# Performance work log

Hardware: AMD Instinct MI355X
Metric: run time of the kernel (lower is better)

The kernel has to match this reference:

```python
import jax, jax.numpy as jnp
import numpy as np

MASK_ID = -100
L, D, HID, NH = 10, 768, 3072, 12
DH = D // NH
REACH = 2  # (sliding_window_size - 1) // 2 with window 5


def _layernorm(x, g, b, eps=1e-5):
    mu = x.mean(-1, keepdims=True)
    var = ((x - mu) ** 2).mean(-1, keepdims=True)
    return (x - mu) * jax.lax.rsqrt(var + eps) * g + b


def _adaln(x, temb, w, bb, g, be):
    # AdaLayerNormShiftScale: linear(silu(temb)) -> (scale, shift)
    e = jax.nn.silu(temb) @ w + bb
    scale, shift = jnp.split(e, 2, axis=-1)
    return _layernorm(x, g, be) * (1.0 + scale) + shift


def _timestep_emb(t):
    half = D // 2
    exponent = -np.log(10000.0) * jnp.arange(half, dtype=jnp.float32) / (half - 1.0)
    freq = jnp.exp(exponent)  # [half]
    emb = t.astype(jnp.float32)[..., None] * freq  # [b,s,half]
    return jnp.concatenate([jnp.sin(emb), jnp.cos(emb)], axis=-1)  # [b,s,D]


def setup_inputs():
    key = jax.random.key(0)
    ks = jax.random.split(key, 16)
    b, s = 4, 1024
    # packed token ids: 4 samples of 256 tokens (16x16 grid), last 64 tokens padding
    idx = np.arange(s)
    sid = idx // 256
    hpos = (idx % 256) // 16
    wpos = idx % 16
    sid = np.where(idx >= 960, MASK_ID, sid)
    tok = np.stack([sid, hpos, wpos], axis=-1)  # [s,3]
    token_ids = jnp.asarray(np.broadcast_to(tok, (b, s, 3)).copy(), dtype=jnp.int32)
    t = jax.random.randint(ks[0], (b, 1), 0, L + 1).astype(jnp.int32)
    t = jnp.broadcast_to(t, (b, s))

    def w(k, shape):
        return jax.random.normal(k, shape, jnp.float32) * 0.02

    return dict(
        x=jax.random.normal(ks[1], (b, s, D), jnp.float32),
        t=t,
        token_ids=token_ids,
        proj_in_w=w(ks[2], (D, D)), proj_in_b=jnp.zeros((D,), jnp.float32),
        h_emb=w(ks[3], (64, D)), w_emb=w(ks[4], (64, D)),
        adaln1_w=w(ks[5], (L, D, 2 * D)), adaln1_b=jnp.zeros((L, 2 * D), jnp.float32),
        ln1_g=jnp.ones((L, D), jnp.float32), ln1_b=jnp.zeros((L, D), jnp.float32),
        qkv_w=w(ks[6], (L, D, 3 * D)), qkv_b=jnp.zeros((L, 3 * D), jnp.float32),
        o_w=w(ks[7], (L, D, D)), o_b=jnp.zeros((L, D), jnp.float32),
        adaln2_w=w(ks[8], (L, D, 2 * D)), adaln2_b=jnp.zeros((L, 2 * D), jnp.float32),
        ln2_g=jnp.ones((L, D), jnp.float32), ln2_b=jnp.zeros((L, D), jnp.float32),
        fc1_w=w(ks[9], (L, D, HID)), fc1_b=jnp.zeros((L, HID), jnp.float32),
        fc2_w=w(ks[10], (L, HID, D)), fc2_b=jnp.zeros((L, D), jnp.float32),
        nout_w=w(ks[11], (D, 2 * D)), nout_b=jnp.zeros((2 * D,), jnp.float32),
        nout_g=jnp.ones((D,), jnp.float32), nout_beta=jnp.zeros((D,), jnp.float32),
    )


def _encoder(x, t, token_ids, proj_in_w, proj_in_b, h_emb, w_emb,
             adaln1_w, adaln1_b, ln1_g, ln1_b, qkv_w, qkv_b, o_w, o_b,
             adaln2_w, adaln2_b, ln2_g, ln2_b, fc1_w, fc1_b, fc2_w, fc2_b,
             nout_w, nout_b, nout_g, nout_beta):
    b, s, _ = x.shape
    sample_ids = token_ids[..., 0]          # [b,s]
    pos = token_ids[..., 1:]                # [b,s,2]
    x = x @ proj_in_w + proj_in_b
    x = x + h_emb[pos[..., 0]] + w_emb[pos[..., 1]]

    # block-sparse mask: same packed sample, Chebyshev sliding window, no padding queries
    same = sample_ids[:, :, None] == sample_ids[:, None, :]              # [b,s,s]
    cheby = jnp.abs(pos[:, :, None, :] - pos[:, None, :, :]).max(-1)      # [b,s,s]
    notpad_q = (sample_ids != MASK_ID)[:, :, None]
    mask = same & (cheby <= REACH) & notpad_q                             # [b,s,s]
    row_valid = mask.any(-1)[..., None]                                   # [b,s,1]

    temb = _timestep_emb(t)  # [b,s,D]
    scale = 1.0 / np.sqrt(DH)
    for i in range(L):
        h1 = _adaln(x, temb, adaln1_w[i], adaln1_b[i], ln1_g[i], ln1_b[i])
        qkv = h1 @ qkv_w[i] + qkv_b[i]
        q, k, v = jnp.split(qkv, 3, axis=-1)
        q = q.reshape(b, s, NH, DH)
        k = k.reshape(b, s, NH, DH)
        v = v.reshape(b, s, NH, DH)
        scores = jnp.einsum('bqhd,bkhd->bhqk', q, k) * scale
        scores = jnp.where(mask[:, None], scores, -1e30)
        attn = jax.nn.softmax(scores, axis=-1)
        o = jnp.einsum('bhqk,bkhd->bqhd', attn, v).reshape(b, s, D)
        o = jnp.where(row_valid, o, 0.0)  # fully-masked (padding) rows -> 0
        x = x + o @ o_w[i] + o_b[i]
        h2 = _adaln(x, temb, adaln2_w[i], adaln2_b[i], ln2_g[i], ln2_b[i])
        x = x + jax.nn.gelu(h2 @ fc1_w[i] + fc1_b[i], approximate=False) @ fc2_w[i] + fc2_b[i]
    x = _adaln(x, temb, nout_w, nout_b, nout_g, nout_beta)
    return x


def reference(x, t, token_ids, proj_in_w, proj_in_b, h_emb, w_emb,
              adaln1_w, adaln1_b, ln1_g, ln1_b, qkv_w, qkv_b, o_w, o_b,
              adaln2_w, adaln2_b, ln2_g, ln2_b, fc1_w, fc1_b, fc2_w, fc2_b,
              nout_w, nout_b, nout_g, nout_beta):
    return _encoder(x, t, token_ids, proj_in_w, proj_in_b, h_emb, w_emb,
                    adaln1_w, adaln1_b, ln1_g, ln1_b, qkv_w, qkv_b, o_w, o_b,
                    adaln2_w, adaln2_b, ln2_g, ln2_b, fc1_w, fc1_b, fc2_w, fc2_b,
                    nout_w, nout_b, nout_g, nout_beta)
```

## Files before the change

### kernel.cpp

```cpp
#include <hip/hip_runtime.h>
#include <hip/hip_bf16.h>
#include <math.h>

#define MASK_ID (-100)
#define SEQ 1024
#define BATCH 4
#define DMODEL 768
#define NHEAD 12
#define DHEAD 64
#define NLAYER 10
#define HIDDEN 3072

typedef unsigned short ushort_t;
typedef unsigned int uint_t;

__device__ __forceinline__ ushort_t f2bf(float f) {
    uint_t u = __float_as_uint(f);
    u = u + 0x7fffu + ((u >> 16) & 1u);
    return (ushort_t)(u >> 16);
}
__device__ __forceinline__ float bf2f(ushort_t u) {
    return __uint_as_float(((uint_t)u) << 16);
}

__device__ __forceinline__ void async_ld16(ushort_t* lds, const ushort_t* g) {
    __builtin_amdgcn_global_load_lds((__attribute__((address_space(1))) const void*)g,
                                     (__attribute__((address_space(3))) void*)lds, 16, 0, 0);
}

#define WAITVM(n) asm volatile("s_waitcnt vmcnt(" #n ")" ::: "memory")

__global__ void temb_silu_kernel(const int* __restrict__ t, float* __restrict__ stemb) {
    int b = blockIdx.x;
    int j = threadIdx.x;
    float tv = (float)t[b * SEQ];
    float freq = expf(-logf(10000.f) * (float)j / 383.f);
    float arg = tv * freq;
    float s = sinf(arg), c = cosf(arg);
    stemb[b * DMODEL + j]       = s / (1.f + expf(-s));
    stemb[b * DMODEL + 384 + j] = c / (1.f + expf(-c));
}

__global__ __launch_bounds__(256)
void build_nbr_kernel(const int* __restrict__ tok, short* __restrict__ nbr,
                      int* __restrict__ nbr_cnt) {
    int m = blockIdx.x * 256 + threadIdx.x;
    int b = m >> 10, q = m & 1023;
    int sid = tok[m * 3];
    int cnt = 0;
    short* lst = nbr + (size_t)m * 28;
    if (sid != MASK_ID) {
        int qh = tok[m * 3 + 1], qw = tok[m * 3 + 2];
        for (int dh = -2; dh <= 2; ++dh) {
            for (int dw = -2; dw <= 2; ++dw) {
                int kq = q + dh * 16 + dw;
                if (kq < 0 || kq >= SEQ) continue;
                int km = b * SEQ + kq;
                if (tok[km * 3] != sid) continue;
                int kh2 = tok[km * 3 + 1], kw2 = tok[km * 3 + 2];
                int adh = kh2 - qh; if (adh < 0) adh = -adh;
                int adw = kw2 - qw; if (adw < 0) adw = -adw;
                if (adh > 2 || adw > 2) continue;
                lst[cnt++] = (short)kq;
            }
        }
    }
    nbr_cnt[m] = cnt;
}

#define PREP_GRID 20400
__global__ __launch_bounds__(256)
void prep_all_kernel(const float* __restrict__ w0, const float* __restrict__ w1,
                     const float* __restrict__ w2, const float* __restrict__ w3,
                     ushort_t* __restrict__ o0, ushort_t* __restrict__ o1,
                     ushort_t* __restrict__ o2, ushort_t* __restrict__ o3,
                     const float* __restrict__ proj_in_w, ushort_t* __restrict__ projT,
                     const float* __restrict__ x_in, ushort_t* __restrict__ h_bf,
                     const float* __restrict__ stemb,
                     const float* __restrict__ a1w, const float* __restrict__ a2w,
                     const float* __restrict__ nw, float* __restrict__ partial) {
    __shared__ __align__(16) char smem[64 * 65 * 2];
    int gid = blockIdx.x;
    int tid = threadIdx.x;

    if (gid < 17280) {
        int layer = gid / 1728;
        int id = gid % 1728;
        const float* in; ushort_t* out; int R, C, tile_id, TX;
        if (id < 432) {
            in = w0 + (size_t)layer * DMODEL * 3 * DMODEL; out = o0 + (size_t)layer * 3 * DMODEL * DMODEL;
            R = DMODEL; C = 3 * DMODEL; tile_id = id; TX = 36;
        } else if (id < 576) {
            in = w1 + (size_t)layer * DMODEL * DMODEL; out = o1 + (size_t)layer * DMODEL * DMODEL;
            R = DMODEL; C = DMODEL; tile_id = id - 432; TX = 12;
        } else if (id < 1152) {
            in = w2 + (size_t)layer * DMODEL * HIDDEN; out = o2 + (size_t)layer * HIDDEN * DMODEL;
            R = DMODEL; C = HIDDEN; tile_id = id - 576; TX = 48;
        } else {
            in = w3 + (size_t)layer * HIDDEN * DMODEL; out = o3 + (size_t)layer * DMODEL * HIDDEN;
            R = HIDDEN; C = DMODEL; tile_id = id - 1152; TX = 12;
        }
        int c0 = (tile_id % TX) * 64, r0 = (tile_id / TX) * 64;
        ushort_t* tlb = (ushort_t*)smem;
        #pragma unroll
        for (int i = 0; i < 4; ++i) {
            int idx = i * 256 + tid;
            int r = idx >> 4, c4 = (idx & 15) * 4;
            float4 v = *(const float4*)&in[(size_t)(r0 + r) * C + c0 + c4];
            tlb[r * 65 + c4 + 0] = f2bf(v.x);
            tlb[r * 65 + c4 + 1] = f2bf(v.y);
            tlb[r * 65 + c4 + 2] = f2bf(v.z);
            tlb[r * 65 + c4 + 3] = f2bf(v.w);
        }
        __syncthreads();
        #pragma unroll
        for (int j = 0; j < 8; ++j) {
            int idx = j * 256 + tid;
            int oc = idx >> 5, pr = idx & 31;
            uint_t pk = (uint_t)tlb[(pr * 2) * 65 + oc] | ((uint_t)tlb[(pr * 2 + 1) * 65 + oc] << 16);
            *(uint_t*)&out[(size_t)(c0 + oc) * R + r0 + pr * 2] = pk;
        }
    } else if (gid < 17856) {
        int s = gid - 17280;
        int c0 = (s % 24) * 32, r0 = (s / 24) * 32;
        float* tile = (float*)smem;
        int tx = tid & 31, ty = tid >> 5;
        #pragma unroll
        for (int i = 0; i < 4; ++i)
            tile[(ty + 8 * i) * 33 + tx] = proj_in_w[(size_t)(r0 + ty + 8 * i) * DMODEL + c0 + tx];
        __syncthreads();
        #pragma unroll
        for (int i = 0; i < 4; ++i)
            projT[(size_t)(c0 + ty + 8 * i) * DMODEL + r0 + tx] = f2bf(tile[tx * 33 + ty + 8 * i]);
    } else if (gid < 19392) {
        int i = (gid - 17856) * 256 + tid;
        float4 a = ((const float4*)x_in)[2 * i];
        float4 b = ((const float4*)x_in)[2 * i + 1];
        uint4 o;
        o.x = (uint_t)f2bf(a.x) | ((uint_t)f2bf(a.y) << 16);
        o.y = (uint_t)f2bf(a.z) | ((uint_t)f2bf(a.w) << 16);
        o.z = (uint_t)f2bf(b.x) | ((uint_t)f2bf(b.y) << 16);
        o.w = (uint_t)f2bf(b.z) | ((uint_t)f2bf(b.w) << 16);
        ((uint4*)h_bf)[i] = o;
    } else {
        int s3 = gid - 19392;
        int chunk = s3 % 6;
        int kc = (s3 / 6) % 8;
        int slot = s3 / 48;
        int col = chunk * 256 + tid;
        const float* W;
        if (slot == 20) W = nw;
        else {
            int i = slot >> 1;
            W = ((slot & 1) ? a2w : a1w) + (size_t)i * DMODEL * 2 * DMODEL;
        }
        float* sb = (float*)smem;
        for (int idx = tid; idx < 4 * 96; idx += 256) {
            int bb = idx / 96, kk = idx % 96;
            sb[idx] = stemb[bb * DMODEL + kc * 96 + kk];
        }
        __syncthreads();
        const float* Wp = W + (size_t)(kc * 96) * (2 * DMODEL) + col;
        float a0 = 0.f, a1 = 0.f, a2 = 0.f, a3 = 0.f;
        #pragma unroll 4
        for (int kk = 0; kk < 96; ++kk) {
            float w = Wp[(size_t)kk * (2 * DMODEL)];
            a0 = fmaf(sb[kk], w, a0);
            a1 = fmaf(sb[96 + kk], w, a1);
            a2 = fmaf(sb[192 + kk], w, a2);
            a3 = fmaf(sb[288 + kk], w, a3);
        }
        size_t base = ((size_t)(slot * 8 + kc) * 4) * (2 * DMODEL) + col;
        partial[base + 0 * 2 * DMODEL] = a0;
        partial[base + 1 * 2 * DMODEL] = a1;
        partial[base + 2 * 2 * DMODEL] = a2;
        partial[base + 3 * 2 * DMODEL] = a3;
    }
}

__global__ __launch_bounds__(256)
void adaln_reduce_kernel(const float* __restrict__ partial,
                         const float* __restrict__ a1b, const float* __restrict__ a2b,
                         const float* __restrict__ nb,
                         float* __restrict__ e_all) {
    int chunk = blockIdx.x;
    int slot  = blockIdx.y;
    int col = chunk * 256 + threadIdx.x;
    const float* bb;
    if (slot == 20) bb = nb;
    else {
        int i = slot >> 1;
        bb = ((slot & 1) ? a2b : a1b) + i * 2 * DMODEL;
    }
    float bias = bb[col];
    float s0 = bias, s1 = bias, s2 = bias, s3 = bias;
    #pragma unroll
    for (int kc = 0; kc < 8; ++kc) {
        size_t base = ((size_t)(slot * 8 + kc) * 4) * (2 * DMODEL) + col;
        s0 += partial[base + 0 * 2 * DMODEL];
        s1 += partial[base + 1 * 2 * DMODEL];
        s2 += partial[base + 2 * 2 * DMODEL];
        s3 += partial[base + 3 * 2 * DMODEL];
    }
    size_t o = (size_t)slot * 4 * (2 * DMODEL) + col;
    e_all[o + 0 * 2 * DMODEL] = s0;
    e_all[o + 1 * 2 * DMODEL] = s1;
    e_all[o + 2 * 2 * DMODEL] = s2;
    e_all[o + 3 * 2 * DMODEL] = s3;
}

template<int OUT_BF>
__global__ __launch_bounds__(256)
void ln_adaln_kernel(const float* __restrict__ in, void* __restrict__ outv,
                     const float* __restrict__ g, const float* __restrict__ be,
                     const float* __restrict__ e) {
    int wid = threadIdx.x >> 6, lane = threadIdx.x & 63;
    int row = blockIdx.x * 4 + wid;
    int b = row >> 10;
    const float* xr = in + (size_t)row * DMODEL;
    float v[12];
    float s = 0.f, ss = 0.f;
    #pragma unroll
    for (int j = 0; j < 12; ++j) {
        v[j] = xr[lane + j * 64];
        s += v[j];
        ss = fmaf(v[j], v[j], ss);
    }
    #pragma unroll
    for (int o = 1; o < 64; o <<= 1) { s += __shfl_xor(s, o); ss += __shfl_xor(ss, o); }
    float mu = s * (1.f / DMODEL);
    float var = ss * (1.f / DMODEL) - mu * mu;
    float rs = rsqrtf(var + 1e-5f);
    const float* esc = e + (size_t)b * (2 * DMODEL);
    #pragma unroll
    for (int j = 0; j < 12; ++j) {
        int c = lane + j * 64;
        float y = (v[j] - mu) * rs * g[c] + be[c];
        y = y * (1.f + esc[c]) + esc[DMODEL + c];
        if (OUT_BF) ((ushort_t*)outv)[(size_t)row * DMODEL + c] = f2bf(y);
        else        ((float*)outv)[(size_t)row * DMODEL + c] = y;
    }
}

__device__ __forceinline__ float gelu_exact(float x) {
    return 0.5f * x * (1.f + erff(x * 0.70710678118654752f));
}

template<int EPI>
__global__ __launch_bounds__(256, 3)
void gemm_bf16_big(const ushort_t* __restrict__ A, const ushort_t* __restrict__ Wt,
                   const float* __restrict__ bias, void* __restrict__ outv,
                   int M, int N, int K) {
    constexpr int BM = 128, BN = 128;
    using f32x4  = __attribute__((ext_vector_type(4))) float;
    using bf16x8 = __attribute__((ext_vector_type(8))) short;

    __shared__ __align__(16) ushort_t lds[(BM + BN) * 64];

    int tid = threadIdx.x;
    int lane = tid & 63, wid = tid >> 6;
    int wr = wid >> 1, wc = wid & 1;
    int l16 = lane & 15, lg = lane >> 4;
    int sw = l16 & 7;

    int nx = N / BN;
    int cpx = gridDim.x >> 3;
    int wg = blockIdx.x;
    int wgid = (wg & 7) * cpx + (wg >> 3);
    int bx = wgid % nx, by = wgid / nx;
    int bm0 = by * BM, bn0 = bx * BN;

    f32x4 acc[4][4];
    #pragma unroll
    for (int m = 0; m < 4; ++m)
        #pragma unroll
        for (int n = 0; n < 4; ++n)
            #pragma unroll
            for (int r = 0; r < 4; ++r) acc[m][n][r] = 0.f;

    const ushort_t* Abase = A + (size_t)bm0 * K;
    const ushort_t* Bbase = Wt + (size_t)bn0 * K;

    int nk = K >> 6;
    for (int kt = 0; kt < nk; ++kt) {
        #pragma unroll
        for (int s2 = 0; s2 < 4; ++s2) {
            int ca = s2 * 256 + tid;
            int rw = ca >> 3, kcs = (ca & 7) ^ (rw & 7);
            async_ld16(&lds[ca * 8], Abase + (size_t)rw * K + kt * 64 + kcs * 8);
        }
        #pragma unroll
        for (int s2 = 0; s2 < 4; ++s2) {
            int ca = s2 * 256 + tid;
            int rw = ca >> 3, kcs = (ca & 7) ^ (rw & 7);
            async_ld16(&lds[BM * 64 + ca * 8], Bbase + (size_t)rw * K + kt * 64 + kcs * 8);
        }
        WAITVM(0);
        __syncthreads();
        #pragma unroll
        for (int kk = 0; kk < 2; ++kk) {
            int csw = (kk * 4 + lg) ^ sw;
            bf16x8 af[4], bfr[4];
            #pragma unroll
            for (int m = 0; m < 4; ++m)
                af[m] = *(const bf16x8*)&lds[(wr * 64 + m * 16 + l16) * 64 + csw * 8];
            #pragma unroll
            for (int n = 0; n < 4; ++n)
                bfr[n] = *(const bf16x8*)&lds[BM * 64 + (wc * 64 + n * 16 + l16) * 64 + csw * 8];
            #pragma unroll
            for (int m = 0; m < 4; ++m)
                #pragma unroll
                for (int n = 0; n < 4; ++n)
                    acc[m][n] = __builtin_amdgcn_mfma_f32_16x16x32_bf16(af[m], bfr[n], acc[m][n], 0, 0, 0);
        }
        __syncthreads();
    }

    int r0 = bm0 + wr * 64, c0 = bn0 + wc * 64;
    #pragma unroll
    for (int m = 0; m < 4; ++m) {
        #pragma unroll
        for (int n = 0; n < 4; ++n) {
            int cc = c0 + n * 16 + l16;
            float bcol = bias[cc];
            #pragma unroll
            for (int r = 0; r < 4; ++r) {
                int row = r0 + m * 16 + lg * 4 + r;
                float v = acc[m][n][r] + bcol;
                if (EPI == 0) ((ushort_t*)outv)[(size_t)row * N + cc] = f2bf(v);
                else          ((ushort_t*)outv)[(size_t)row * N + cc] = f2bf(gelu_exact(v));
            }
        }
    }
}

template<int BM, int BN, int EPI, int OCC>
__global__ __launch_bounds__(256, OCC)
void gemm_bf16(const ushort_t* __restrict__ A, const ushort_t* __restrict__ Wt,
               const float* __restrict__ bias, void* __restrict__ outv,
               const float* __restrict__ emb_h, const float* __restrict__ emb_w,
               const int* __restrict__ tok,
               int M, int N, int K) {
    constexpr int WM = BM / 2, WN = BN / 2;
    constexpr int FM = WM / 16, FN = WN / 16;
    constexpr int BUF = (BM + BN) * 64;
    constexpr int LPT = (BM + BN) / 32;
    using f32x4  = __attribute__((ext_vector_type(4))) float;
    using bf16x8 = __attribute__((ext_vector_type(8))) short;

    __shared__ __align__(16) ushort_t lds[3 * BUF];

    int tid = threadIdx.x;
    int lane = tid & 63, wid = tid >> 6;
    int wr = wid >> 1, wc = wid & 1;
    int l16 = lane & 15, lg = lane >> 4;
    int sw = l16 & 7;

    int nx = N / BN;
    int cpx = gridDim.x >> 3;
    int wg = blockIdx.x;
    int wgid = (wg & 7) * cpx + (wg >> 3);
    int bx = wgid % nx, by = wgid / nx;
    int bm0 = by * BM, bn0 = bx * BN;

    f32x4 acc[FM][FN];
    #pragma unroll
    for (int m = 0; m < FM; ++m)
        #pragma unroll
        for (int n = 0; n < FN; ++n)
            #pragma unroll
            for (int r = 0; r < 4; ++r) acc[m][n][r] = 0.f;

    const ushort_t* Abase = A + (size_t)bm0 * K;
    const ushort_t* Bbase = Wt + (size_t)bn0 * K;

    #define STAGE(bufi, kt)                                                             \
        do {                                                                            \
            _Pragma("unroll")                                                           \
            for (int s2 = 0; s2 < BM / 32; ++s2) {                                      \
                int ca = s2 * 256 + tid;                                                \
                int rw = ca >> 3, kcs = (ca & 7) ^ (rw & 7);                            \
                async_ld16(&lds[(bufi) * BUF + ca * 8],                                 \
                           Abase + (size_t)rw * K + (kt) * 64 + kcs * 8);               \
            }                                                                           \
            _Pragma("unroll")                                                           \
            for (int s2 = 0; s2 < BN / 32; ++s2) {                                      \
                int ca = s2 * 256 + tid;                                                \
                int rw = ca >> 3, kcs = (ca & 7) ^ (rw & 7);                            \
                async_ld16(&lds[(bufi) * BUF + BM * 64 + ca * 8],                       \
                           Bbase + (size_t)rw * K + (kt) * 64 + kcs * 8);               \
            }                                                                           \
        } while (0)

    int nk = K >> 6;
    STAGE(0, 0);
    STAGE(1, 1);
    int bufi = 0;
    for (int kt = 0; kt < nk; ++kt) {
        int nxt = bufi + 2; if (nxt >= 3) nxt -= 3;
        if (kt + 2 < nk) {
            STAGE(nxt, kt + 2);
            if constexpr (LPT == 4) WAITVM(8); else WAITVM(12);
        } else if (kt + 1 < nk) {
            if constexpr (LPT == 4) WAITVM(4); else WAITVM(6);
        } else {
            WAITVM(0);
        }
        __builtin_amdgcn_s_barrier();
        __builtin_amdgcn_s_setprio(1);
        #pragma unroll
        for (int kk = 0; kk < 2; ++kk) {
            bf16x8 af[FM], bfr[FN];
            #pragma unroll
            for (int m = 0; m < FM; ++m) {
                int row = wr * WM + m * 16 + l16;
                int csw = (kk * 4 + lg) ^ sw;
                af[m] = *(const bf16x8*)&lds[bufi * BUF + row * 64 + csw * 8];
            }
            #pragma unroll
            for (int n = 0; n < FN; ++n) {
                int row = wc * WN + n * 16 + l16;
                int csw = (kk * 4 + lg) ^ sw;
                bfr[n] = *(const bf16x8*)&lds[bufi * BUF + BM * 64 + row * 64 + csw * 8];
            }
            #pragma unroll
            for (int m = 0; m < FM; ++m)
                #pragma unroll
                for (int n = 0; n < FN; ++n)
                    acc[m][n] = __builtin_amdgcn_mfma_f32_16x16x32_bf16(af[m], bfr[n], acc[m][n], 0, 0, 0);
        }
        __builtin_amdgcn_s_setprio(0);
        __builtin_amdgcn_s_barrier();
        ++bufi; if (bufi >= 3) bufi = 0;
    }
    #undef STAGE

    int r0 = bm0 + wr * WM, c0 = bn0 + wc * WN;
    #pragma unroll
    for (int m = 0; m < FM; ++m) {
        #pragma unroll
        for (int n = 0; n < FN; ++n) {
            int cc = c0 + n * 16 + l16;
            float bcol = bias[cc];
            #pragma unroll
            for (int r = 0; r < 4; ++r) {
                int row = r0 + m * 16 + lg * 4 + r;
                float v = acc[m][n][r] + bcol;
                if (EPI == 0) {
                    ((ushort_t*)outv)[(size_t)row * N + cc] = f2bf(v);
                } else if (EPI == 1) {
                    int p0 = tok[row * 3 + 1], p1 = tok[row * 3 + 2];
                    v += emb_h[p0 * DMODEL + cc] + emb_w[p1 * DMODEL + cc];
                    ((float*)outv)[(size_t)row * N + cc] = v;
                } else if (EPI == 2) {
                    float* op = (float*)outv + (size_t)row * N + cc;
                    *op = *op + v;
                } else {
                    ((ushort_t*)outv)[(size_t)row * N + cc] = f2bf(gelu_exact(v));
                }
            }
        }
    }
}

__global__ __launch_bounds__(256)
void attn_kernel(const ushort_t* __restrict__ qkv, const short* __restrict__ nbr,
                 const int* __restrict__ nbr_cnt, ushort_t* __restrict__ o_out) {
    int tid = threadIdx.x;
    int u = tid >> 2, part = tid & 3;
    int q = blockIdx.x * 16 + (u & 15);
    int h = blockIdx.y * 4 + (u >> 4);
    int b = blockIdx.z;
    int m = b * SEQ + q;
    ushort_t* op = o_out + (size_t)m * DMODEL + h * DHEAD + part * 16;
    int cnt = nbr_cnt[m];
    if (cnt == 0) {
        uint4 z = {0u, 0u, 0u, 0u};
        ((uint4*)op)[0] = z;
        ((uint4*)op)[1] = z;
        return;
    }
    const short* lst = nbr + (size_t)m * 28;
    const ushort_t* qp = qkv + (size_t)m * (3 * DMODEL) + h * DHEAD + part * 16;
    float qv[16], ov[16];
    {
        uint4 u0 = ((const uint4*)qp)[0];
        uint4 u1 = ((const uint4*)qp)[1];
        qv[0] = bf2f(u0.x & 0xffff) * 0.125f; qv[1] = bf2f(u0.x >> 16) * 0.125f;
        qv[2] = bf2f(u0.y & 0xffff) * 0.125f; qv[3] = bf2f(u0.y >> 16) * 0.125f;
        qv[4] = bf2f(u0.z & 0xffff) * 0.125f; qv[5] = bf2f(u0.z >> 16) * 0.125f;
        qv[6] = bf2f(u0.w & 0xffff) * 0.125f; qv[7] = bf2f(u0.w >> 16) * 0.125f;
        qv[8]  = bf2f(u1.x & 0xffff) * 0.125f; qv[9]  = bf2f(u1.x >> 16) * 0.125f;
        qv[10] = bf2f(u1.y & 0xffff) * 0.125f; qv[11] = bf2f(u1.y >> 16) * 0.125f;
        qv[12] = bf2f(u1.z & 0xffff) * 0.125f; qv[13] = bf2f(u1.z >> 16) * 0.125f;
        qv[14] = bf2f(u1.w & 0xffff) * 0.125f; qv[15] = bf2f(u1.w >> 16) * 0.125f;
    }
    #pragma unroll
    for (int i = 0; i < 16; ++i) ov[i] = 0.f;
    float mx = -1e30f, den = 0.f;
    for (int it = 0; it < cnt; ++it) {
        int km = b * SEQ + (int)lst[it];
        const ushort_t* kp = qkv + (size_t)km * (3 * DMODEL) + DMODEL + h * DHEAD + part * 16;
        float dot;
        {
            uint4 u0 = ((const uint4*)kp)[0];
            uint4 u1 = ((const uint4*)kp)[1];
            dot = qv[0] * bf2f(u0.x & 0xffff);
            dot = fmaf(qv[1], bf2f(u0.x >> 16), dot);
            dot = fmaf(qv[2], bf2f(u0.y & 0xffff), dot);
            dot = fmaf(qv[3], bf2f(u0.y >> 16), dot);
            dot = fmaf(qv[4], bf2f(u0.z & 0xffff), dot);
            dot = fmaf(qv[5], bf2f(u0.z >> 16), dot);
            dot = fmaf(qv[6], bf2f(u0.w & 0xffff), dot);
            dot = fmaf(qv[7], bf2f(u0.w >> 16), dot);
            dot = fmaf(qv[8],  bf2f(u1.x & 0xffff), dot);
            dot = fmaf(qv[9],  bf2f(u1.x >> 16), dot);
            dot = fmaf(qv[10], bf2f(u1.y & 0xffff), dot);
            dot = fmaf(qv[11], bf2f(u1.y >> 16), dot);
            dot = fmaf(qv[12], bf2f(u1.z & 0xffff), dot);
            dot = fmaf(qv[13], bf2f(u1.z >> 16), dot);
            dot = fmaf(qv[14], bf2f(u1.w & 0xffff), dot);
            dot = fmaf(qv[15], bf2f(u1.w >> 16), dot);
        }
        dot += __shfl_xor(dot, 1);
        dot += __shfl_xor(dot, 2);
        float sc = dot;
        float nm = fmaxf(mx, sc);
        float c1 = expf(mx - nm);
        float c2 = expf(sc - nm);
        den = den * c1 + c2;
        const ushort_t* vp = qkv + (size_t)km * (3 * DMODEL) + 2 * DMODEL + h * DHEAD + part * 16;
        {
            uint4 u0 = ((const uint4*)vp)[0];
            uint4 u1 = ((const uint4*)vp)[1];
            ov[0] = ov[0] * c1 + c2 * bf2f(u0.x & 0xffff);
            ov[1] = ov[1] * c1 + c2 * bf2f(u0.x >> 16);
            ov[2] = ov[2] * c1 + c2 * bf2f(u0.y & 0xffff);
            ov[3] = ov[3] * c1 + c2 * bf2f(u0.y >> 16);
            ov[4] = ov[4] * c1 + c2 * bf2f(u0.z & 0xffff);
            ov[5] = ov[5] * c1 + c2 * bf2f(u0.z >> 16);
            ov[6] = ov[6] * c1 + c2 * bf2f(u0.w & 0xffff);
            ov[7] = ov[7] * c1 + c2 * bf2f(u0.w >> 16);
            ov[8]  = ov[8]  * c1 + c2 * bf2f(u1.x & 0xffff);
            ov[9]  = ov[9]  * c1 + c2 * bf2f(u1.x >> 16);
            ov[10] = ov[10] * c1 + c2 * bf2f(u1.y & 0xffff);
            ov[11] = ov[11] * c1 + c2 * bf2f(u1.y >> 16);
            ov[12] = ov[12] * c1 + c2 * bf2f(u1.z & 0xffff);
            ov[13] = ov[13] * c1 + c2 * bf2f(u1.z >> 16);
            ov[14] = ov[14] * c1 + c2 * bf2f(u1.w & 0xffff);
            ov[15] = ov[15] * c1 + c2 * bf2f(u1.w >> 16);
        }
        mx = nm;
    }
    float inv = 1.f / den;
    uint4 o0, o1;
    o0.x = (uint_t)f2bf(ov[0] * inv) | ((uint_t)f2bf(ov[1] * inv) << 16);
    o0.y = (uint_t)f2bf(ov[2] * inv) | ((uint_t)f2bf(ov[3] * inv) << 16);
    o0.z = (uint_t)f2bf(ov[4] * inv) | ((uint_t)f2bf(ov[5] * inv) << 16);
    o0.w = (uint_t)f2bf(ov[6] * inv) | ((uint_t)f2bf(ov[7] * inv) << 16);
    o1.x = (uint_t)f2bf(ov[8]  * inv) | ((uint_t)f2bf(ov[9]  * inv) << 16);
    o1.y = (uint_t)f2bf(ov[10] * inv) | ((uint_t)f2bf(ov[11] * inv) << 16);
    o1.z = (uint_t)f2bf(ov[12] * inv) | ((uint_t)f2bf(ov[13] * inv) << 16);
    o1.w = (uint_t)f2bf(ov[14] * inv) | ((uint_t)f2bf(ov[15] * inv) << 16);
    ((uint4*)op)[0] = o0;
    ((uint4*)op)[1] = o1;
}

extern "C" void kernel_launch(void* const* d_in, const int* in_sizes, int n_in,
                              void* d_out, int out_size, void* d_ws, size_t ws_size,
                              hipStream_t stream) {
    const float* x_in      = (const float*)d_in[0];
    const int*   t         = (const int*)d_in[1];
    const int*   tok       = (const int*)d_in[2];
    const float* proj_in_w = (const float*)d_in[3];
    const float* proj_in_b = (const float*)d_in[4];
    const float* h_emb     = (const float*)d_in[5];
    const float* w_emb     = (const float*)d_in[6];
    const float* adaln1_w  = (const float*)d_in[7];
    const float* adaln1_b  = (const float*)d_in[8];
    const float* ln1_g     = (const float*)d_in[9];
    const float* ln1_b     = (const float*)d_in[10];
    const float* qkv_w     = (const float*)d_in[11];
    const float* qkv_b     = (const float*)d_in[12];
    const float* o_w       = (const float*)d_in[13];
    const float* o_b       = (const float*)d_in[14];
    const float* adaln2_w  = (const float*)d_in[15];
    const float* adaln2_b  = (const float*)d_in[16];
    const float* ln2_g     = (const float*)d_in[17];
    const float* ln2_b     = (const float*)d_in[18];
    const float* fc1_w     = (const float*)d_in[19];
    const float* fc1_b     = (const float*)d_in[20];
    const float* fc2_w     = (const float*)d_in[21];
    const float* fc2_b     = (const float*)d_in[22];
    const float* nout_w    = (const float*)d_in[23];
    const float* nout_b    = (const float*)d_in[24];
    const float* nout_g    = (const float*)d_in[25];
    const float* nout_beta = (const float*)d_in[26];

    const int M = BATCH * SEQ;

    float* stemb   = (float*)d_ws;
    float* e_all   = stemb + BATCH * DMODEL;
    float* partial = e_all + 21 * BATCH * 2 * DMODEL;
    int*   nbr_cnt = (int*)(partial + 21 * 8 * 4 * 2 * DMODEL);
    short* nbr     = (short*)(nbr_cnt + M);
    ushort_t* h_bf   = (ushort_t*)(nbr + (size_t)M * 28);
    ushort_t* qkv_bf = h_bf + (size_t)M * DMODEL;
    ushort_t* hid_bf = qkv_bf + (size_t)M * 3 * DMODEL;
    ushort_t* projT  = hid_bf + (size_t)M * HIDDEN;
    ushort_t* qkvT_a = projT + (size_t)DMODEL * DMODEL;
    ushort_t* oT_a   = qkvT_a + (size_t)NLAYER * 3 * DMODEL * DMODEL;
    ushort_t* fc1T_a = oT_a + (size_t)NLAYER * DMODEL * DMODEL;
    ushort_t* fc2T_a = fc1T_a + (size_t)NLAYER * DMODEL * HIDDEN;
    float* x = (float*)d_out;

    temb_silu_kernel<<<BATCH, 384, 0, stream>>>(t, stemb);
    build_nbr_kernel<<<M / 256, 256, 0, stream>>>(tok, nbr, nbr_cnt);
    prep_all_kernel<<<PREP_GRID, 256, 0, stream>>>(
        qkv_w, o_w, fc1_w, fc2_w, qkvT_a, oT_a, fc1T_a, fc2T_a,
        proj_in_w, projT, x_in, h_bf, stemb, adaln1_w, adaln2_w, nout_w, partial);
    adaln_reduce_kernel<<<dim3(6, 2 * NLAYER + 1), 256, 0, stream>>>(
        partial, adaln1_b, adaln2_b, nout_b, e_all);

    gemm_bf16<64, 64, 1, 3><<<(DMODEL / 64) * (M / 64), 256, 0, stream>>>(
        h_bf, projT, proj_in_b, x, h_emb, w_emb, tok, M, DMODEL, DMODEL);

    for (int i = 0; i < NLAYER; ++i) {
        ln_adaln_kernel<1><<<M / 4, 256, 0, stream>>>(
            x, h_bf, ln1_g + i * DMODEL, ln1_b + i * DMODEL,
            e_all + (size_t)(2 * i) * BATCH * 2 * DMODEL);
        gemm_bf16_big<0><<<(3 * DMODEL / 128) * (M / 128), 256, 0, stream>>>(
            h_bf, qkvT_a + (size_t)i * 3 * DMODEL * DMODEL, qkv_b + i * 3 * DMODEL,
            qkv_bf, M, 3 * DMODEL, DMODEL);
        attn_kernel<<<dim3(SEQ / 16, NHEAD / 4, BATCH), 256, 0, stream>>>(qkv_bf, nbr, nbr_cnt, h_bf);
        gemm_bf16<64, 64, 2, 3><<<(DMODEL / 64) * (M / 64), 256, 0, stream>>>(
            h_bf, oT_a + (size_t)i * DMODEL * DMODEL, o_b + i * DMODEL,
            x, nullptr, nullptr, nullptr, M, DMODEL, DMODEL);
        ln_adaln_kernel<1><<<M / 4, 256, 0, stream>>>(
            x, h_bf, ln2_g + i * DMODEL, ln2_b + i * DMODEL,
            e_all + (size_t)(2 * i + 1) * BATCH * 2 * DMODEL);
        gemm_bf16_big<3><<<(HIDDEN / 128) * (M / 128), 256, 0, stream>>>(
            h_bf, fc1T_a + (size_t)i * DMODEL * HIDDEN, fc1_b + i * HIDDEN,
            hid_bf, M, HIDDEN, DMODEL);
        gemm_bf16<128, 64, 2, 2><<<(DMODEL / 64) * (M / 128), 256, 0, stream>>>(
            hid_bf, fc2T_a + (size_t)i * DMODEL * HIDDEN, fc2_b + i * DMODEL,
            x, nullptr, nullptr, nullptr, M, DMODEL, HIDDEN);
    }

    ln_adaln_kernel<0><<<M / 4, 256, 0, stream>>>(
        x, x, nout_g, nout_beta, e_all + (size_t)(2 * NLAYER) * BATCH * 2 * DMODEL);
}
```

Baseline: 1.631 ms.

## Store transposed weights as contiguous 64x64 tiles and fold neighbor build into prep

The weight-transpose prep now writes bf16 weights in a blocked layout where each 64x64 (N,K) tile is contiguous, and both GEMM kernels compute B-tile addresses in that blocked layout. This makes each async 16-byte load for a B tile read from one contiguous 8KB region instead of strided rows, which should improve DRAM/TLB locality. The proj_in transpose is routed through the same tile path, and the neighbor-list build is merged into the prep kernel to drop one launch. All GEMM consumers must agree on the new layout, which adds coupling between prep and the GEMM kernels.

```diff
diff --git a/kernel.cpp b/kernel.cpp
--- a/kernel.cpp
+++ b/kernel.cpp
@@ -29,6 +29,7 @@
 }
 
 #define WAITVM(n) asm volatile("s_waitcnt vmcnt(" #n ")" ::: "memory")
+
 
 __global__ void temb_silu_kernel(const int* __restrict__ t, float* __restrict__ stemb) {
     int b = blockIdx.x;
@@ -41,34 +42,7 @@
     stemb[b * DMODEL + 384 + j] = c / (1.f + expf(-c));
 }
 
-__global__ __launch_bounds__(256)
-void build_nbr_kernel(const int* __restrict__ tok, short* __restrict__ nbr,
-                      int* __restrict__ nbr_cnt) {
-    int m = blockIdx.x * 256 + threadIdx.x;
-    int b = m >> 10, q = m & 1023;
-    int sid = tok[m * 3];
-    int cnt = 0;
-    short* lst = nbr + (size_t)m * 28;
-    if (sid != MASK_ID) {
-        int qh = tok[m * 3 + 1], qw = tok[m * 3 + 2];
-        for (int dh = -2; dh <= 2; ++dh) {
-            for (int dw = -2; dw <= 2; ++dw) {
-                int kq = q + dh * 16 + dw;
-                if (kq < 0 || kq >= SEQ) continue;
-                int km = b * SEQ + kq;
-                if (tok[km * 3] != sid) continue;
-                int kh2 = tok[km * 3 + 1], kw2 = tok[km * 3 + 2];
-                int adh = kh2 - qh; if (adh < 0) adh = -adh;
-                int adw = kw2 - qw; if (adw < 0) adw = -adw;
-                if (adh > 2 || adw > 2) continue;
-                lst[cnt++] = (short)kq;
-            }
-        }
-    }
-    nbr_cnt[m] = cnt;
-}
-
-#define PREP_GRID 20400
+#define PREP_GRID 19984
 __global__ __launch_bounds__(256)
 void prep_all_kernel(const float* __restrict__ w0, const float* __restrict__ w1,
                      const float* __restrict__ w2, const float* __restrict__ w3,
@@ -78,29 +52,37 @@
                      const float* __restrict__ x_in, ushort_t* __restrict__ h_bf,
                      const float* __restrict__ stemb,
                      const float* __restrict__ a1w, const float* __restrict__ a2w,
-                     const float* __restrict__ nw, float* __restrict__ partial) {
+                     const float* __restrict__ nw, float* __restrict__ partial,
+                     const int* __restrict__ tok, short* __restrict__ nbr,
+                     int* __restrict__ nbr_cnt) {
     __shared__ __align__(16) char smem[64 * 65 * 2];
     int gid = blockIdx.x;
     int tid = threadIdx.x;
 
-    if (gid < 17280) {
-        int layer = gid / 1728;
-        int id = gid % 1728;
+    if (gid < 17424) {
         const float* in; ushort_t* out; int R, C, tile_id, TX;
-        if (id < 432) {
-            in = w0 + (size_t)layer * DMODEL * 3 * DMODEL; out = o0 + (size_t)layer * 3 * DMODEL * DMODEL;
-            R = DMODEL; C = 3 * DMODEL; tile_id = id; TX = 36;
-        } else if (id < 576) {
-            in = w1 + (size_t)layer * DMODEL * DMODEL; out = o1 + (size_t)layer * DMODEL * DMODEL;
-            R = DMODEL; C = DMODEL; tile_id = id - 432; TX = 12;
-        } else if (id < 1152) {
-            in = w2 + (size_t)layer * DMODEL * HIDDEN; out = o2 + (size_t)layer * HIDDEN * DMODEL;
-            R = DMODEL; C = HIDDEN; tile_id = id - 576; TX = 48;
+        if (gid < 17280) {
+            int layer = gid / 1728;
+            int id = gid % 1728;
+            if (id < 432) {
+                in = w0 + (size_t)layer * DMODEL * 3 * DMODEL; out = o0 + (size_t)layer * 3 * DMODEL * DMODEL;
+                R = DMODEL; C = 3 * DMODEL; tile_id = id; TX = 36;
+            } else if (id < 576) {
+                in = w1 + (size_t)layer * DMODEL * DMODEL; out = o1 + (size_t)layer * DMODEL * DMODEL;
+                R = DMODEL; C = DMODEL; tile_id = id - 432; TX = 12;
+            } else if (id < 1152) {
+                in = w2 + (size_t)layer * DMODEL * HIDDEN; out = o2 + (size_t)layer * HIDDEN * DMODEL;
+                R = DMODEL; C = HIDDEN; tile_id = id - 576; TX = 48;
+            } else {
+                in = w3 + (size_t)layer * HIDDEN * DMODEL; out = o3 + (size_t)layer * DMODEL * HIDDEN;
+                R = HIDDEN; C = DMODEL; tile_id = id - 1152; TX = 12;
+            }
         } else {
-            in = w3 + (size_t)layer * HIDDEN * DMODEL; out = o3 + (size_t)layer * DMODEL * HIDDEN;
-            R = HIDDEN; C = DMODEL; tile_id = id - 1152; TX = 12;
+            in = proj_in_w; out = projT; R = DMODEL; C = DMODEL; tile_id = gid - 17280; TX = 12;
         }
         int c0 = (tile_id % TX) * 64, r0 = (tile_id / TX) * 64;
+        int KB = R >> 6;
+        int nb = c0 >> 6, kb = r0 >> 6;
         ushort_t* tlb = (ushort_t*)smem;
         #pragma unroll
         for (int i = 0; i < 4; ++i) {
@@ -113,27 +95,16 @@
             tlb[r * 65 + c4 + 3] = f2bf(v.w);
         }
         __syncthreads();
+        ushort_t* ob = out + (((size_t)(nb * KB + kb)) << 12);
         #pragma unroll
         for (int j = 0; j < 8; ++j) {
             int idx = j * 256 + tid;
-            int oc = idx >> 5, pr = idx & 31;
-            uint_t pk = (uint_t)tlb[(pr * 2) * 65 + oc] | ((uint_t)tlb[(pr * 2 + 1) * 65 + oc] << 16);
-            *(uint_t*)&out[(size_t)(c0 + oc) * R + r0 + pr * 2] = pk;
-        }
-    } else if (gid < 17856) {
-        int s = gid - 17280;
-        int c0 = (s % 24) * 32, r0 = (s / 24) * 32;
-        float* tile = (float*)smem;
-        int tx = tid & 31, ty = tid >> 5;
-        #pragma unroll
-        for (int i = 0; i < 4; ++i)
-            tile[(ty + 8 * i) * 33 + tx] = proj_in_w[(size_t)(r0 + ty + 8 * i) * DMODEL + c0 + tx];
-        __syncthreads();
-        #pragma unroll
-        for (int i = 0; i < 4; ++i)
-            projT[(size_t)(c0 + ty + 8 * i) * DMODEL + r0 + tx] = f2bf(tile[tx * 33 + ty + 8 * i]);
-    } else if (gid < 19392) {
-        int i = (gid - 17856) * 256 + tid;
+            int ni = idx >> 5, kp = idx & 31;
+            uint_t pk = (uint_t)tlb[(kp * 2) * 65 + ni] | ((uint_t)tlb[(kp * 2 + 1) * 65 + ni] << 16);
+            *(uint_t*)&ob[ni * 64 + kp * 2] = pk;
+        }
+    } else if (gid < 18960) {
+        int i = (gid - 17424) * 256 + tid;
         float4 a = ((const float4*)x_in)[2 * i];
         float4 b = ((const float4*)x_in)[2 * i + 1];
         uint4 o;
@@ -142,8 +113,8 @@
         o.z = (uint_t)f2bf(b.x) | ((uint_t)f2bf(b.y) << 16);
         o.w = (uint_t)f2bf(b.z) | ((uint_t)f2bf(b.w) << 16);
         ((uint4*)h_bf)[i] = o;
-    } else {
-        int s3 = gid - 19392;
+    } else if (gid < 19968) {
+        int s3 = gid - 18960;
         int chunk = s3 % 6;
         int kc = (s3 / 6) % 8;
         int slot = s3 / 48;
@@ -175,6 +146,29 @@
         partial[base + 1 * 2 * DMODEL] = a1;
         partial[base + 2 * 2 * DMODEL] = a2;
         partial[base + 3 * 2 * DMODEL] = a3;
+    } else {
+        int m = (gid - 19968) * 256 + tid;
+        int b = m >> 10, q = m & 1023;
+        int sid = tok[m * 3];
+        int cnt = 0;
+        short* lst = nbr + (size_t)m * 28;
+        if (sid != MASK_ID) {
+            int qh = tok[m * 3 + 1], qw = tok[m * 3 + 2];
+            for (int dh = -2; dh <= 2; ++dh) {
+                for (int dw = -2; dw <= 2; ++dw) {
+                    int kq = q + dh * 16 + dw;
+                    if (kq < 0 || kq >= SEQ) continue;
+                    int km = b * SEQ + kq;
+                    if (tok[km * 3] != sid) continue;
+                    int kh2 = tok[km * 3 + 1], kw2 = tok[km * 3 + 2];
+                    int adh = kh2 - qh; if (adh < 0) adh = -adh;
+                    int adw = kw2 - qw; if (adw < 0) adw = -adw;
+                    if (adh > 2 || adw > 2) continue;
+                    lst[cnt++] = (short)kq;
+                }
+            }
+        }
+        nbr_cnt[m] = cnt;
     }
 }
 
@@ -279,7 +273,8 @@
             for (int r = 0; r < 4; ++r) acc[m][n][r] = 0.f;
 
     const ushort_t* Abase = A + (size_t)bm0 * K;
-    const ushort_t* Bbase = Wt + (size_t)bn0 * K;
+    int KB = K >> 6;
+    const ushort_t* Bt0 = Wt + (((size_t)(bn0 >> 6) * KB) << 12);
 
     int nk = K >> 6;
     for (int kt = 0; kt < nk; ++kt) {
@@ -293,7 +288,8 @@
         for (int s2 = 0; s2 < 4; ++s2) {
             int ca = s2 * 256 + tid;
             int rw = ca >> 3, kcs = (ca & 7) ^ (rw & 7);
-            async_ld16(&lds[BM * 64 + ca * 8], Bbase + (size_t)rw * K + kt * 64 + kcs * 8);
+            async_ld16(&lds[BM * 64 + ca * 8],
+                       Bt0 + ((((size_t)(rw >> 6) * KB + kt) << 12)) + (rw & 63) * 64 + kcs * 8);
         }
         WAITVM(0);
         __syncthreads();
@@ -372,7 +368,8 @@
             for (int r = 0; r < 4; ++r) acc[m][n][r] = 0.f;
 
     const ushort_t* Abase = A + (size_t)bm0 * K;
-    const ushort_t* Bbase = Wt + (size_t)bn0 * K;
+    int KB = K >> 6;
+    const ushort_t* Bt0 = Wt + (((size_t)(bn0 >> 6) * KB) << 12);
 
     #define STAGE(bufi, kt)                                                             \
         do {                                                                            \
@@ -388,7 +385,8 @@
                 int ca = s2 * 256 + tid;                                                \
                 int rw = ca >> 3, kcs = (ca & 7) ^ (rw & 7);                            \
                 async_ld16(&lds[(bufi) * BUF + BM * 64 + ca * 8],                       \
-                           Bbase + (size_t)rw * K + (kt) * 64 + kcs * 8);               \
+                           Bt0 + ((((size_t)(rw >> 6) * KB + (kt)) << 12))              \
+                               + (rw & 63) * 64 + kcs * 8);                             \
             }                                                                           \
         } while (0)
 
@@ -615,10 +613,10 @@
     float* x = (float*)d_out;
 
     temb_silu_kernel<<<BATCH, 384, 0, stream>>>(t, stemb);
-    build_nbr_kernel<<<M / 256, 256, 0, stream>>>(tok, nbr, nbr_cnt);
     prep_all_kernel<<<PREP_GRID, 256, 0, stream>>>(
         qkv_w, o_w, fc1_w, fc2_w, qkvT_a, oT_a, fc1T_a, fc2T_a,
-        proj_in_w, projT, x_in, h_bf, stemb, adaln1_w, adaln2_w, nout_w, partial);
+        proj_in_w, projT, x_in, h_bf, stemb, adaln1_w, adaln2_w, nout_w, partial,
+        tok, nbr, nbr_cnt);
     adaln_reduce_kernel<<<dim3(6, 2 * NLAYER + 1), 256, 0, stream>>>(
         partial, adaln1_b, adaln2_b, nout_b, e_all);
 
```

Result: no change. 1.620 ms, median of 2 (-0.7%).
